# Optimization experiments

Measured on AMD Instinct MI355X. Metric: run time of the kernel, lower is better.

The kernel has to match this reference:

```python
import jax, jax.numpy as jnp
import numpy as np

N = 100000      # nodes
E = 1600000     # edges (avg degree 16)
IN = 128        # in_channels
OUT = 64        # out_channels
EDGE_DIM = 16   # edge_attr feature dim (ignored: edge_dim=None in TransformerConv)


def _lin_params(key, fan_in, fan_out):
    kw, kb = jax.random.split(key)
    bound = 1.0 / np.sqrt(fan_in)
    W = jax.random.uniform(kw, (fan_in, fan_out), minval=-bound, maxval=bound, dtype=jnp.float32)
    b = jax.random.uniform(kb, (fan_out,), minval=-bound, maxval=bound, dtype=jnp.float32)
    return W, b


def setup_inputs() -> dict:
    key = jax.random.key(0)
    ks = jax.random.split(key, 11)
    x = jax.random.normal(ks[0], (N, IN), dtype=jnp.float32)
    edge_index = jax.random.randint(ks[1], (2, E), 0, N, dtype=jnp.int64)
    edge_attr = jax.random.normal(ks[2], (E, EDGE_DIM), dtype=jnp.float32)
    Wq1, bq1 = _lin_params(ks[3], IN, OUT)
    Wk1, bk1 = _lin_params(ks[4], IN, OUT)
    Wv1, bv1 = _lin_params(ks[5], IN, OUT)
    Ws1, bs1 = _lin_params(ks[6], IN, OUT)
    Wq2, bq2 = _lin_params(ks[7], OUT, OUT)
    Wk2, bk2 = _lin_params(ks[8], OUT, OUT)
    Wv2, bv2 = _lin_params(ks[9], OUT, OUT)
    Ws2, bs2 = _lin_params(ks[10], OUT, OUT)
    return dict(x=x, edge_index=edge_index, edge_attr=edge_attr,
                Wq1=Wq1, bq1=bq1, Wk1=Wk1, bk1=bk1, Wv1=Wv1, bv1=bv1, Ws1=Ws1, bs1=bs1,
                Wq2=Wq2, bq2=bq2, Wk2=Wk2, bk2=bk2, Wv2=Wv2, bv2=bv2, Ws2=Ws2, bs2=bs2)


def _transformer_conv(x, src, dst, Wq, bq, Wk, bk, Wv, bv, Ws, bs):
    # heads=1 PyG TransformerConv, edge_dim=None (edge_attr ignored)
    C = Wq.shape[1]
    q = x @ Wq + bq                     # [N, C] queries (target side)
    k = x @ Wk + bk                     # [N, C] keys (source side)
    v = x @ Wv + bv                     # [N, C] values (source side)
    # per-edge attention logit: q_i . k_j / sqrt(C)  (i = dst, j = src)
    scores = jnp.sum(q[dst] * k[src], axis=-1) / jnp.sqrt(jnp.float32(C))  # [E]
    # segment softmax over incoming edges of each destination node
    seg_max = jax.ops.segment_max(scores, dst, num_segments=N)             # [N]
    seg_max = jnp.where(jnp.isfinite(seg_max), seg_max, 0.0)
    ex = jnp.exp(scores - seg_max[dst])                                    # [E]
    seg_sum = jax.ops.segment_sum(ex, dst, num_segments=N)                 # [N]
    alpha = ex / jnp.maximum(seg_sum[dst], 1e-16)                          # [E]
    # scatter-aggregate weighted values, plus root/skip connection
    msg = alpha[:, None] * v[src]                                          # [E, C]
    agg = jax.ops.segment_sum(msg, dst, num_segments=N)                    # [N, C]
    return agg + (x @ Ws + bs)


def reference(x, edge_index, edge_attr,
              Wq1, bq1, Wk1, bk1, Wv1, bv1, Ws1, bs1,
              Wq2, bq2, Wk2, bk2, Wv2, bv2, Ws2, bs2):
    src, dst = edge_index[0], edge_index[1]
    h = _transformer_conv(x, src, dst, Wq1, bq1, Wk1, bk1, Wv1, bv1, Ws1, bs1)
    h = jax.nn.relu(h)
    out = _transformer_conv(h, src, dst, Wq2, bq2, Wk2, bk2, Wv2, bv2, Ws2, bs2)
    return out
```

## Files before the change

kernel.cpp:

```cpp
#include <hip/hip_runtime.h>

typedef __attribute__((ext_vector_type(8))) short short8;
typedef __attribute__((ext_vector_type(4))) float f32x4;

__device__ __forceinline__ unsigned short f2bf(float f) {
    unsigned u = __float_as_uint(f);
    unsigned r = (u + 0x7fff + ((u >> 16) & 1)) >> 16;
    return (unsigned short)r;
}
__device__ __forceinline__ float bf2f(unsigned short h) {
    return __uint_as_float(((unsigned)h) << 16);
}
__device__ __forceinline__ float bflo(unsigned u) { return __uint_as_float(u << 16); }
__device__ __forceinline__ float bfhi(unsigned u) { return __uint_as_float(u & 0xffff0000u); }


#define NB1 64

__global__ __launch_bounds__(256) void k_sort1a(const int* __restrict__ dst, int E, int chunk,
                                                int* __restrict__ hist1) {
    __shared__ int h[256];
    int b = blockIdx.x, t = threadIdx.x;
    h[t] = 0;
    __syncthreads();
    int start = b * chunk, end = min(start + chunk, E);
    for (int i = start + t; i < end; i += 256) atomicAdd(&h[dst[i] >> 9], 1);
    __syncthreads();
    hist1[b * 256 + t] = h[t];
}

__global__ __launch_bounds__(256) void k_sort1b(int* __restrict__ hist1, int* __restrict__ bOff,
                                                int E) {
    __shared__ int tot[256];
    __shared__ int sc[256];
    int t = threadIdx.x;
    int run = 0;
    for (int b = 0; b < NB1; ++b) {
        int idx = b * 256 + t;
        int c = hist1[idx];
        hist1[idx] = run;
        run += c;
    }
    tot[t] = run;
    sc[t] = run;
    __syncthreads();
    for (int off = 1; off < 256; off <<= 1) {
        int x = (t >= off) ? sc[t - off] : 0;
        __syncthreads();
        sc[t] += x;
        __syncthreads();
    }
    bOff[t] = sc[t] - tot[t];
    if (t == 0) bOff[256] = E;
}

__global__ __launch_bounds__(256) void k_sort1c(const int* __restrict__ src,
                                                const int* __restrict__ dst, int E, int chunk,
                                                const int* __restrict__ hist1,
                                                const int* __restrict__ bOff,
                                                int2* __restrict__ buf1) {
    __shared__ int cur[256];
    int b = blockIdx.x, t = threadIdx.x;
    cur[t] = hist1[b * 256 + t];
    __syncthreads();
    int start = b * chunk, end = min(start + chunk, E);
    for (int i = start + t; i < end; i += 256) {
        int d = dst[i];
        int bkt = d >> 9;
        int r = atomicAdd(&cur[bkt], 1);
        buf1[bOff[bkt] + r] = make_int2(d, src[i]);
    }
}

__global__ __launch_bounds__(256) void k_sort2(const int2* __restrict__ buf1,
                                               const int* __restrict__ bOff,
                                               int* __restrict__ rowptr, int* __restrict__ csr,
                                               int n, int E) {
    __shared__ int cnt[512];
    __shared__ int scn[512];
    __shared__ int part[256];
    int b = blockIdx.x, t = threadIdx.x;
    int lo = bOff[b], hi = bOff[b + 1];
    cnt[t] = 0;
    cnt[t + 256] = 0;
    __syncthreads();
    for (int i = lo + t; i < hi; i += 256) atomicAdd(&cnt[buf1[i].x & 511], 1);
    __syncthreads();
    int a0 = cnt[2 * t], a1 = cnt[2 * t + 1];
    part[t] = a0 + a1;
    __syncthreads();
    for (int off = 1; off < 256; off <<= 1) {
        int x = (t >= off) ? part[t - off] : 0;
        __syncthreads();
        part[t] += x;
        __syncthreads();
    }
    int excl = part[t] - (a0 + a1);
    scn[2 * t] = excl;
    scn[2 * t + 1] = excl + a0;
    __syncthreads();
    int node0 = b << 9;
    for (int j = t; j < 512; j += 256) {
        int node = node0 + j;
        if (node < n) rowptr[node] = lo + scn[j];
    }
    if (b == 0 && t == 0) rowptr[n] = E;
    cnt[t] = 0;
    cnt[t + 256] = 0;
    __syncthreads();
    for (int i = lo + t; i < hi; i += 256) {
        int2 e = buf1[i];
        int d = e.x & 511;
        int r = atomicAdd(&cnt[d], 1);
        csr[lo + scn[d] + r] = e.y;
    }
}


__global__ void k_cvtX(const float* __restrict__ X, unsigned short* __restrict__ Xbf, int total4) {
    int i = blockIdx.x * blockDim.x + threadIdx.x;
    if (i < total4) {
        float4 v = *(const float4*)(X + (size_t)i * 4);
        ushort4 o;
        o.x = f2bf(v.x); o.y = f2bf(v.y); o.z = f2bf(v.z); o.w = f2bf(v.w);
        *(ushort4*)(Xbf + (size_t)i * 4) = o;
    }
}

__global__ void k_cvtW(const float* __restrict__ W0, const float* __restrict__ W1,
                       const float* __restrict__ W2, const float* __restrict__ W3,
                       unsigned short* __restrict__ WT, int K) {
    int idx = blockIdx.x * blockDim.x + threadIdx.x;
    int tot = 4 * 64 * K;
    if (idx >= tot) return;
    int slot = idx / (64 * K);
    int rem = idx % (64 * K);
    int j = rem / K, k = rem % K;
    const float* W = (slot == 0) ? W0 : (slot == 1) ? W1 : (slot == 2) ? W2 : W3;
    WT[idx] = f2bf(W[k * 64 + j]);
}


template <int K>
__global__ __launch_bounds__(256) void k_gemm_mfma(
    const unsigned short* __restrict__ Xbf, int n,
    const unsigned short* __restrict__ WT,
    const float* __restrict__ b0, const float* __restrict__ b1,
    const float* __restrict__ b2, const float* __restrict__ b3,
    void* __restrict__ O0, void* __restrict__ O1,
    void* __restrict__ O2, void* __restrict__ O3) {
    const int slot = blockIdx.y;
    const float* B = (slot == 0) ? b0 : (slot == 1) ? b1 : (slot == 2) ? b2 : b3;
    void* O = (slot == 0) ? O0 : (slot == 1) ? O1 : (slot == 2) ? O2 : O3;
    const bool isbf = (slot == 1 || slot == 2);

    __shared__ unsigned short xs[64 * K];
    __shared__ unsigned short ws[64 * K];
    const int t = threadIdx.x;
    const int row0 = blockIdx.x * 64;
    const int K2 = K * 2;
    const int CPR = K / 8;

    const unsigned short* wslot = WT + (size_t)slot * 64 * K;
    for (int c = t; c < 64 * CPR; c += 256) {
        int row = c / CPR, chunk = c % CPR;
        int grow = row0 + row;
        uint4 v = make_uint4(0, 0, 0, 0);
        if (grow < n) v = *(const uint4*)(Xbf + (size_t)grow * K + chunk * 8);
        int byte = (row * K2 + chunk * 16) ^ ((row & 7) << 4);
        *(uint4*)((char*)xs + byte) = v;
        uint4 wv = *(const uint4*)(wslot + (size_t)row * K + chunk * 8);
        *(uint4*)((char*)ws + byte) = wv;
    }
    __syncthreads();

    const int w = t >> 6, l = t & 63;
    const int lr = l & 15, lg = l >> 4;
    f32x4 acc[4];
#pragma unroll
    for (int j = 0; j < 4; ++j) acc[j] = (f32x4){0.f, 0.f, 0.f, 0.f};

#pragma unroll
    for (int ks = 0; ks < K / 32; ++ks) {
        int kb_ = (ks * 32 + lg * 8) * 2;
        int arow = w * 16 + lr;
        short8 a = *(const short8*)((char*)xs + ((arow * K2 + kb_) ^ ((arow & 7) << 4)));
#pragma unroll
        for (int j = 0; j < 4; ++j) {
            int brow = j * 16 + lr;
            short8 b = *(const short8*)((char*)ws + ((brow * K2 + kb_) ^ ((brow & 7) << 4)));
            acc[j] = __builtin_amdgcn_mfma_f32_16x16x32_bf16(a, b, acc[j], 0, 0, 0);
        }
    }

#pragma unroll
    for (int j = 0; j < 4; ++j) {
        int col = j * 16 + lr;
        float bv = B[col];
#pragma unroll
        for (int r = 0; r < 4; ++r) {
            int grow = row0 + w * 16 + lg * 4 + r;
            if (grow < n) {
                float val = acc[j][r] + bv;
                if (isbf) ((unsigned short*)O)[(size_t)grow * 64 + col] = f2bf(val);
                else      ((float*)O)[(size_t)grow * 64 + col] = val;
            }
        }
    }
}


__global__ __launch_bounds__(256) void k_attn(
    const float* __restrict__ q, const unsigned short* __restrict__ kk,
    const unsigned short* __restrict__ vv,
    const float* __restrict__ skip, const int* __restrict__ rowptr, const int* __restrict__ csr,
    void* __restrict__ out, int n, int dorelu, int obf) {
    int wid = threadIdx.x >> 6, lane = threadIdx.x & 63;
    int node = blockIdx.x * 4 + wid;
    if (node >= n) return;
    int start = rowptr[node];
    int deg = rowptr[node + 1] - start;
    int g = lane >> 3;
    int cl = lane & 7;
    const float* qrow = q + (size_t)node * 64 + cl * 8;
    float4 qa = *(const float4*)qrow;
    float4 qb_ = *(const float4*)(qrow + 4);
    float a0 = 0.f, a1 = 0.f, a2 = 0.f, a3 = 0.f, a4 = 0.f, a5 = 0.f, a6 = 0.f, a7 = 0.f;
    float sumex = 0.f;
#pragma unroll 2
    for (int j0 = 0; j0 < deg; j0 += 8) {
        int jj = j0 + g;
        bool act = jj < deg;
        int s_ = act ? csr[start + jj] : 0;
        uint4 kr = *(const uint4*)(kk + (size_t)s_ * 64 + cl * 8);
        float d = qa.x * bflo(kr.x) + qa.y * bfhi(kr.x) + qa.z * bflo(kr.y) + qa.w * bfhi(kr.y) +
                  qb_.x * bflo(kr.z) + qb_.y * bfhi(kr.z) + qb_.z * bflo(kr.w) + qb_.w * bfhi(kr.w);
        d += __shfl_xor(d, 1);
        d += __shfl_xor(d, 2);
        d += __shfl_xor(d, 4);
        float ex = act ? __expf(d * 0.125f) : 0.f;
        sumex += ex;
        uint4 vr = *(const uint4*)(vv + (size_t)s_ * 64 + cl * 8);
        a0 += ex * bflo(vr.x); a1 += ex * bfhi(vr.x);
        a2 += ex * bflo(vr.y); a3 += ex * bfhi(vr.y);
        a4 += ex * bflo(vr.z); a5 += ex * bfhi(vr.z);
        a6 += ex * bflo(vr.w); a7 += ex * bfhi(vr.w);
    }
#define RED3(v) v += __shfl_xor(v, 8); v += __shfl_xor(v, 16); v += __shfl_xor(v, 32);
    RED3(a0) RED3(a1) RED3(a2) RED3(a3) RED3(a4) RED3(a5) RED3(a6) RED3(a7) RED3(sumex)
#undef RED3
    if (g == 0) {
        float r = 1.0f / fmaxf(sumex, 1e-16f);
        const float* srow = skip + (size_t)node * 64 + cl * 8;
        float4 sa = *(const float4*)srow;
        float4 sb = *(const float4*)(srow + 4);
        float o0 = a0 * r + sa.x, o1 = a1 * r + sa.y, o2 = a2 * r + sa.z, o3 = a3 * r + sa.w;
        float o4 = a4 * r + sb.x, o5 = a5 * r + sb.y, o6 = a6 * r + sb.z, o7 = a7 * r + sb.w;
        if (dorelu) {
            o0 = fmaxf(o0, 0.f); o1 = fmaxf(o1, 0.f); o2 = fmaxf(o2, 0.f); o3 = fmaxf(o3, 0.f);
            o4 = fmaxf(o4, 0.f); o5 = fmaxf(o5, 0.f); o6 = fmaxf(o6, 0.f); o7 = fmaxf(o7, 0.f);
        }
        if (obf) {
            uint4 st;
            st.x = (unsigned)f2bf(o0) | ((unsigned)f2bf(o1) << 16);
            st.y = (unsigned)f2bf(o2) | ((unsigned)f2bf(o3) << 16);
            st.z = (unsigned)f2bf(o4) | ((unsigned)f2bf(o5) << 16);
            st.w = (unsigned)f2bf(o6) | ((unsigned)f2bf(o7) << 16);
            *(uint4*)((unsigned short*)out + (size_t)node * 64 + cl * 8) = st;
        } else {
            float* orow = (float*)out + (size_t)node * 64 + cl * 8;
            *(float4*)orow = make_float4(o0, o1, o2, o3);
            *(float4*)(orow + 4) = make_float4(o4, o5, o6, o7);
        }
    }
}


extern "C" void kernel_launch(void* const* d_in, const int* in_sizes, int n_in,
                              void* d_out, int out_size, void* d_ws, size_t ws_size,
                              hipStream_t stream) {
    const float* x = (const float*)d_in[0];
    const int* ei = (const int*)d_in[1];
    const float* Wq1 = (const float*)d_in[3];  const float* bq1 = (const float*)d_in[4];
    const float* Wk1 = (const float*)d_in[5];  const float* bk1 = (const float*)d_in[6];
    const float* Wv1 = (const float*)d_in[7];  const float* bv1 = (const float*)d_in[8];
    const float* Ws1 = (const float*)d_in[9];  const float* bs1 = (const float*)d_in[10];
    const float* Wq2 = (const float*)d_in[11]; const float* bq2 = (const float*)d_in[12];
    const float* Wk2 = (const float*)d_in[13]; const float* bk2 = (const float*)d_in[14];
    const float* Wv2 = (const float*)d_in[15]; const float* bv2 = (const float*)d_in[16];
    const float* Ws2 = (const float*)d_in[17]; const float* bs2 = (const float*)d_in[18];

    const int N = in_sizes[0] / 128;
    const int E = in_sizes[1] / 2;
    const int* srcI = ei;
    const int* dstI = ei + E;

    char* w = (char*)d_ws;
    auto alloc = [&](size_t bytes) {
        void* p = (void*)w;
        w += (bytes + 255) & ~(size_t)255;
        return p;
    };
    int* hist1  = (int*)alloc((size_t)NB1 * 256 * 4);
    int* bOff   = (int*)alloc(257 * 4);
    int2* buf1  = (int2*)alloc((size_t)E * 8);
    int* rowptr = (int*)alloc((size_t)(N + 1) * 4);
    int* csr    = (int*)alloc((size_t)E * 4);
    float* qb          = (float*)alloc((size_t)N * 64 * 4);
    unsigned short* kb = (unsigned short*)alloc((size_t)N * 64 * 2);
    unsigned short* vb = (unsigned short*)alloc((size_t)N * 64 * 2);
    float* sb          = (float*)alloc((size_t)N * 64 * 4);
    unsigned short* xbf = (unsigned short*)alloc((size_t)N * 128 * 2);
    unsigned short* hbf = xbf;
    unsigned short* WT1 = (unsigned short*)alloc((size_t)4 * 64 * 128 * 2);
    unsigned short* WT2 = (unsigned short*)alloc((size_t)4 * 64 * 64 * 2);

    const int chunk = (E + NB1 - 1) / NB1;
    const int nbuk = (N + 511) >> 9;

    k_sort1a<<<NB1, 256, 0, stream>>>(dstI, E, chunk, hist1);
    k_sort1b<<<1, 256, 0, stream>>>(hist1, bOff, E);
    k_sort1c<<<NB1, 256, 0, stream>>>(srcI, dstI, E, chunk, hist1, bOff, buf1);
    k_sort2<<<nbuk, 256, 0, stream>>>(buf1, bOff, rowptr, csr, N, E);

    k_cvtX<<<((N * 128 / 4) + 255) / 256, 256, 0, stream>>>(x, xbf, N * 128 / 4);
    k_cvtW<<<(4 * 64 * 128 + 255) / 256, 256, 0, stream>>>(Wq1, Wk1, Wv1, Ws1, WT1, 128);
    k_cvtW<<<(4 * 64 * 64 + 255) / 256, 256, 0, stream>>>(Wq2, Wk2, Wv2, Ws2, WT2, 64);

    dim3 gg((N + 63) / 64, 4);
    k_gemm_mfma<128><<<gg, 256, 0, stream>>>(xbf, N, WT1, bq1, bk1, bv1, bs1,
                                             qb, kb, vb, sb);
    k_attn<<<(N + 3) / 4, 256, 0, stream>>>(qb, kb, vb, sb, rowptr, csr, hbf, N, 1, 1);
    k_gemm_mfma<64><<<gg, 256, 0, stream>>>(hbf, N, WT2, bq2, bk2, bv2, bs2,
                                            qb, kb, vb, sb);
    k_attn<<<(N + 3) / 4, 256, 0, stream>>>(qb, kb, vb, sb, rowptr, csr, d_out, N, 0, 0);
}
```

Before: 537.2 us.

## Redesign CSR bucket sort with many blocks, global atomic offsets, finer buckets

Restructures the destination-sorting (CSR build) phase. The first pass now uses many small chunks, about 1042 blocks instead of 64, and accumulates a global histogram with atomics. The scatter pass claims per-block bucket ranges through global atomic cursors. Buckets shrink from 512 to 128 nodes, which gives 782 second-pass blocks instead of 196, and the second-pass scan is smaller. The goal is to fix low occupancy in the sort kernels, which ran only 64 blocks. In exchange the edge order within a bucket becomes nondeterministic, and there are more global atomics plus an extra memset.

```diff
diff --git a/kernel.cpp b/kernel.cpp
--- a/kernel.cpp
+++ b/kernel.cpp
@@ -15,60 +15,81 @@
 __device__ __forceinline__ float bfhi(unsigned u) { return __uint_as_float(u & 0xffff0000u); }
 
 
-#define NB1 64
-
-__global__ __launch_bounds__(256) void k_sort1a(const int* __restrict__ dst, int E, int chunk,
-                                                int* __restrict__ hist1) {
-    __shared__ int h[256];
+#define BSH 7
+#define NBUK_MAX 1024
+#define CHUNK_MAX 1536
+
+__global__ __launch_bounds__(256) void k_histA(const int* __restrict__ dst, int E, int chunk,
+                                               int nbuk, int* __restrict__ tot) {
+    __shared__ int h[NBUK_MAX];
     int b = blockIdx.x, t = threadIdx.x;
-    h[t] = 0;
+    for (int j = t; j < NBUK_MAX; j += 256) h[j] = 0;
     __syncthreads();
     int start = b * chunk, end = min(start + chunk, E);
-    for (int i = start + t; i < end; i += 256) atomicAdd(&h[dst[i] >> 9], 1);
-    __syncthreads();
-    hist1[b * 256 + t] = h[t];
-}
-
-__global__ __launch_bounds__(256) void k_sort1b(int* __restrict__ hist1, int* __restrict__ bOff,
-                                                int E) {
-    __shared__ int tot[256];
-    __shared__ int sc[256];
+    for (int i = start + t; i < end; i += 256) atomicAdd(&h[dst[i] >> BSH], 1);
+    __syncthreads();
+    for (int j = t; j < nbuk; j += 256) {
+        int v = h[j];
+        if (v) atomicAdd(&tot[j], v);
+    }
+}
+
+__global__ __launch_bounds__(256) void k_scanB(const int* __restrict__ tot, int* __restrict__ bOff,
+                                               int* __restrict__ gcur, int nbuk, int E) {
+    __shared__ int s[256];
     int t = threadIdx.x;
-    int run = 0;
-    for (int b = 0; b < NB1; ++b) {
-        int idx = b * 256 + t;
-        int c = hist1[idx];
-        hist1[idx] = run;
-        run += c;
-    }
-    tot[t] = run;
-    sc[t] = run;
+    int base = t * 4;
+    int v0 = (base + 0 < nbuk) ? tot[base + 0] : 0;
+    int v1 = (base + 1 < nbuk) ? tot[base + 1] : 0;
+    int v2 = (base + 2 < nbuk) ? tot[base + 2] : 0;
+    int v3 = (base + 3 < nbuk) ? tot[base + 3] : 0;
+    int ts = v0 + v1 + v2 + v3;
+    s[t] = ts;
     __syncthreads();
     for (int off = 1; off < 256; off <<= 1) {
-        int x = (t >= off) ? sc[t - off] : 0;
+        int x = (t >= off) ? s[t - off] : 0;
         __syncthreads();
-        sc[t] += x;
+        s[t] += x;
         __syncthreads();
     }
-    bOff[t] = sc[t] - tot[t];
-    if (t == 0) bOff[256] = E;
-}
-
-__global__ __launch_bounds__(256) void k_sort1c(const int* __restrict__ src,
-                                                const int* __restrict__ dst, int E, int chunk,
-                                                const int* __restrict__ hist1,
-                                                const int* __restrict__ bOff,
-                                                int2* __restrict__ buf1) {
-    __shared__ int cur[256];
+    int excl = s[t] - ts;
+    int e0 = excl, e1 = excl + v0, e2 = excl + v0 + v1, e3 = excl + v0 + v1 + v2;
+    if (base + 0 < nbuk) { bOff[base + 0] = e0; gcur[base + 0] = e0; }
+    if (base + 1 < nbuk) { bOff[base + 1] = e1; gcur[base + 1] = e1; }
+    if (base + 2 < nbuk) { bOff[base + 2] = e2; gcur[base + 2] = e2; }
+    if (base + 3 < nbuk) { bOff[base + 3] = e3; gcur[base + 3] = e3; }
+    if (t == 0) bOff[nbuk] = E;
+}
+
+__global__ __launch_bounds__(256) void k_scatB(const int* __restrict__ src,
+                                               const int* __restrict__ dst, int E, int chunk,
+                                               int nbuk, int* __restrict__ gcur,
+                                               int2* __restrict__ buf1) {
+    __shared__ int ldst[CHUNK_MAX];
+    __shared__ int h[NBUK_MAX];
+    __shared__ int bas[NBUK_MAX];
     int b = blockIdx.x, t = threadIdx.x;
-    cur[t] = hist1[b * 256 + t];
+    for (int j = t; j < NBUK_MAX; j += 256) h[j] = 0;
     __syncthreads();
     int start = b * chunk, end = min(start + chunk, E);
     for (int i = start + t; i < end; i += 256) {
         int d = dst[i];
-        int bkt = d >> 9;
-        int r = atomicAdd(&cur[bkt], 1);
-        buf1[bOff[bkt] + r] = make_int2(d, src[i]);
+        ldst[i - start] = d;
+        atomicAdd(&h[d >> BSH], 1);
+    }
+    __syncthreads();
+    for (int j = t; j < nbuk; j += 256) {
+        int c = h[j];
+        if (c) bas[j] = atomicAdd(&gcur[j], c);
+    }
+    __syncthreads();
+    for (int j = t; j < NBUK_MAX; j += 256) h[j] = 0;
+    __syncthreads();
+    for (int i = start + t; i < end; i += 256) {
+        int d = ldst[i - start];
+        int bkt = d >> BSH;
+        int r = atomicAdd(&h[bkt], 1);
+        buf1[bas[bkt] + r] = make_int2(d, src[i]);
     }
 }
 
@@ -76,43 +97,38 @@
                                                const int* __restrict__ bOff,
                                                int* __restrict__ rowptr, int* __restrict__ csr,
                                                int n, int E) {
-    __shared__ int cnt[512];
-    __shared__ int scn[512];
-    __shared__ int part[256];
+    __shared__ int cnt[128];
+    __shared__ int exc[128];
+    __shared__ int sc[128];
     int b = blockIdx.x, t = threadIdx.x;
     int lo = bOff[b], hi = bOff[b + 1];
-    cnt[t] = 0;
-    cnt[t + 256] = 0;
-    __syncthreads();
-    for (int i = lo + t; i < hi; i += 256) atomicAdd(&cnt[buf1[i].x & 511], 1);
-    __syncthreads();
-    int a0 = cnt[2 * t], a1 = cnt[2 * t + 1];
-    part[t] = a0 + a1;
-    __syncthreads();
-    for (int off = 1; off < 256; off <<= 1) {
-        int x = (t >= off) ? part[t - off] : 0;
+    if (t < 128) cnt[t] = 0;
+    __syncthreads();
+    for (int i = lo + t; i < hi; i += 256) atomicAdd(&cnt[buf1[i].x & 127], 1);
+    __syncthreads();
+    int c0 = (t < 128) ? cnt[t] : 0;
+    if (t < 128) sc[t] = c0;
+    __syncthreads();
+    for (int off = 1; off < 128; off <<= 1) {
+        int x = (t < 128 && t >= off) ? sc[t - off] : 0;
         __syncthreads();
-        part[t] += x;
+        if (t < 128) sc[t] += x;
         __syncthreads();
     }
-    int excl = part[t] - (a0 + a1);
-    scn[2 * t] = excl;
-    scn[2 * t + 1] = excl + a0;
-    __syncthreads();
-    int node0 = b << 9;
-    for (int j = t; j < 512; j += 256) {
-        int node = node0 + j;
-        if (node < n) rowptr[node] = lo + scn[j];
+    if (t < 128) {
+        int e = sc[t] - c0;
+        exc[t] = e;
+        int node = (b << BSH) + t;
+        if (node < n) rowptr[node] = lo + e;
+        cnt[t] = 0;
     }
     if (b == 0 && t == 0) rowptr[n] = E;
-    cnt[t] = 0;
-    cnt[t + 256] = 0;
     __syncthreads();
     for (int i = lo + t; i < hi; i += 256) {
         int2 e = buf1[i];
-        int d = e.x & 511;
-        int r = atomicAdd(&cnt[d], 1);
-        csr[lo + scn[d] + r] = e.y;
+        int bin = e.x & 127;
+        int r = atomicAdd(&cnt[bin], 1);
+        csr[lo + exc[bin] + r] = e.y;
     }
 }
 
@@ -301,8 +317,9 @@
         w += (bytes + 255) & ~(size_t)255;
         return p;
     };
-    int* hist1  = (int*)alloc((size_t)NB1 * 256 * 4);
-    int* bOff   = (int*)alloc(257 * 4);
+    int* tot    = (int*)alloc((size_t)NBUK_MAX * 4);
+    int* bOff   = (int*)alloc((size_t)(NBUK_MAX + 1) * 4);
+    int* gcur   = (int*)alloc((size_t)NBUK_MAX * 4);
     int2* buf1  = (int2*)alloc((size_t)E * 8);
     int* rowptr = (int*)alloc((size_t)(N + 1) * 4);
     int* csr    = (int*)alloc((size_t)E * 4);
@@ -315,12 +332,15 @@
     unsigned short* WT1 = (unsigned short*)alloc((size_t)4 * 64 * 128 * 2);
     unsigned short* WT2 = (unsigned short*)alloc((size_t)4 * 64 * 64 * 2);
 
+    const int nbuk = (N + ((1 << BSH) - 1)) >> BSH;
+    const int NB1 = (E + (CHUNK_MAX - 1)) / CHUNK_MAX;
     const int chunk = (E + NB1 - 1) / NB1;
-    const int nbuk = (N + 511) >> 9;
-
-    k_sort1a<<<NB1, 256, 0, stream>>>(dstI, E, chunk, hist1);
-    k_sort1b<<<1, 256, 0, stream>>>(hist1, bOff, E);
-    k_sort1c<<<NB1, 256, 0, stream>>>(srcI, dstI, E, chunk, hist1, bOff, buf1);
+
+    hipMemsetAsync(tot, 0, (size_t)NBUK_MAX * 4, stream);
+
+    k_histA<<<NB1, 256, 0, stream>>>(dstI, E, chunk, nbuk, tot);
+    k_scanB<<<1, 256, 0, stream>>>(tot, bOff, gcur, nbuk, E);
+    k_scatB<<<NB1, 256, 0, stream>>>(srcI, dstI, E, chunk, nbuk, gcur, buf1);
     k_sort2<<<nbuk, 256, 0, stream>>>(buf1, bOff, rowptr, csr, N, E);
 
     k_cvtX<<<((N * 128 / 4) + 255) / 256, 256, 0, stream>>>(x, xbf, N * 128 / 4);
```

After: 497.1 us. 1.08x faster.
